# Performance work log

Hardware: AMD Instinct MI355X
Metric: run time of the kernel (lower is better)

## Reference

```python
import jax, jax.numpy as jnp
import numpy as np

NSLICES = 4
HID = 512
IN_FEAT = 342   # input_shape - 1 (last column is phase)
OUT = 311
BATCH = 256


def cubic(y0, y1, y2, y3, mu):
    # Catmull-Rom cubic interpolation, as in the original PFNN code
    return (
        (-0.5 * y0 + 1.5 * y1 - 1.5 * y2 + 0.5 * y3) * mu * mu * mu
        + (y0 - 2.5 * y1 + 2.0 * y2 - 0.5 * y3) * mu * mu
        + (-0.5 * y0 + 0.5 * y2) * mu
        + y1
    )


def setup_inputs() -> dict:
    key = jax.random.key(0)
    ks = jax.random.split(key, 7)
    x = jax.random.uniform(ks[0], (BATCH, IN_FEAT + 1), dtype=jnp.float32)
    s = 0.02
    W0 = jax.random.normal(ks[1], (NSLICES, HID, IN_FEAT), dtype=jnp.float32) * s
    b0 = jax.random.normal(ks[2], (NSLICES, HID), dtype=jnp.float32) * s
    W1 = jax.random.normal(ks[3], (NSLICES, HID, HID), dtype=jnp.float32) * s
    b1 = jax.random.normal(ks[4], (NSLICES, HID), dtype=jnp.float32) * s
    W2 = jax.random.normal(ks[5], (NSLICES, OUT, HID), dtype=jnp.float32) * s
    b2 = jax.random.normal(ks[6], (NSLICES, OUT), dtype=jnp.float32) * s
    return {"x": x, "W0": W0, "b0": b0, "W1": W1, "b1": b1, "W2": W2, "b2": b2}


def reference(x, W0, b0, W1, b1, W2, b2):
    phase = x[:, -1]                       # [B]
    pscale = NSLICES * phase
    mu = jnp.mod(pscale, 1.0)              # [B]
    i1 = jnp.floor(pscale).astype(jnp.int32) % NSLICES
    i0 = (i1 - 1) % NSLICES
    i2 = (i1 + 1) % NSLICES
    i3 = (i1 + 2) % NSLICES
    muW = mu[:, None, None]                # broadcast over (out, in)
    mub = mu[:, None]

    Wb0 = cubic(W0[i0], W0[i1], W0[i2], W0[i3], muW)   # [B, 512, 342]
    bb0 = cubic(b0[i0], b0[i1], b0[i2], b0[i3], mub)   # [B, 512]
    Wb1 = cubic(W1[i0], W1[i1], W1[i2], W1[i3], muW)   # [B, 512, 512]
    bb1 = cubic(b1[i0], b1[i1], b1[i2], b1[i3], mub)
    Wb2 = cubic(W2[i0], W2[i1], W2[i2], W2[i3], muW)   # [B, 311, 512]
    bb2 = cubic(b2[i0], b2[i1], b2[i2], b2[i3], mub)

    h = x[:, :-1]                                       # [B, 342]
    h = jax.nn.elu(jnp.einsum('boi,bi->bo', Wb0, h) + bb0)
    h = jax.nn.elu(jnp.einsum('boi,bi->bo', Wb1, h) + bb1)
    out = jnp.einsum('boi,bi->bo', Wb2, h) + bb2        # [B, 311]
    return out
```

## Files before the change

### kernel.cpp

```cpp
#include <hip/hip_runtime.h>
#include <math.h>

#define NSLICES 4
#define HID 512
#define IN_FEAT 342
#define OUTD 311
#define BATCH 256
#define KP0 352
#define MP2 320
#define XROW (IN_FEAT + 1)

typedef unsigned short u16;
typedef short bf16x8 __attribute__((ext_vector_type(8)));
typedef float f32x4 __attribute__((ext_vector_type(4)));

__device__ __forceinline__ u16 f2bf_rne(float v) {
    unsigned int x = __float_as_uint(v);
    unsigned int r = (x + 0x7fffu + ((x >> 16) & 1u)) >> 16;
    return (u16)r;
}
__device__ __forceinline__ float bf2f(u16 u) {
    return __uint_as_float(((unsigned int)u) << 16);
}

__global__ __launch_bounds__(64) void prep_x(const float* __restrict__ x,
                                             u16* __restrict__ hhi, u16* __restrict__ hlo,
                                             float* __restrict__ dcoef)
{
    const int b = blockIdx.x;
    const float* xr = x + (size_t)b * XROW;
    for (int k = threadIdx.x; k < KP0; k += 64) {
        float v = (k < IN_FEAT) ? xr[k] : 0.f;
        u16 hi = f2bf_rne(v);
        u16 lo = f2bf_rne(v - bf2f(hi));
        hhi[(size_t)b * KP0 + k] = hi;
        hlo[(size_t)b * KP0 + k] = lo;
    }
    if (threadIdx.x == 0) {
        float ps = 4.f * xr[IN_FEAT];
        float fl = floorf(ps);
        float mu = ps - fl;
        int i1 = ((int)fl) & 3;
        float mu2 = mu * mu, mu3 = mu2 * mu;
        float c0 = -0.5f * mu3 + mu2 - 0.5f * mu;
        float c1 = 1.5f * mu3 - 2.5f * mu2 + 1.0f;
        float c2 = -1.5f * mu3 + 2.0f * mu2 + 0.5f * mu;
        float c3 = 0.5f * mu3 - 0.5f * mu2;
        float d[4];
        d[(i1 + 3) & 3] = c0;
        d[i1]           = c1;
        d[(i1 + 1) & 3] = c2;
        d[(i1 + 2) & 3] = c3;
        float* dd = dcoef + b * 4;
        dd[0] = d[0]; dd[1] = d[1]; dd[2] = d[2]; dd[3] = d[3];
    }
}

#define C0 (4 * 512 * 44)
#define C1 (4 * 512 * 64)
#define C2 (4 * 320 * 64)

union U8 { u16 u[8]; uint4 v; };

__global__ __launch_bounds__(256) void prep_w(
    const float* __restrict__ W0, const float* __restrict__ W1, const float* __restrict__ W2,
    u16* __restrict__ whi0, u16* __restrict__ wlo0,
    u16* __restrict__ whi1, u16* __restrict__ wlo1,
    u16* __restrict__ whi2, u16* __restrict__ wlo2)
{
    int i = blockIdx.x * 256 + threadIdx.x;
    float src[8];
    u16* dhi; u16* dlo; size_t doff;
    if (i < C0) {
        int row = i / 44, c = i - row * 44;
        int k = c * 8;
#pragma unroll
        for (int j = 0; j < 8; j++) {
            int kk = k + j;
            src[j] = (kk < IN_FEAT) ? W0[(size_t)row * IN_FEAT + kk] : 0.f;
        }
        dhi = whi0; dlo = wlo0; doff = (size_t)row * KP0 + k;
    } else if (i < C0 + C1) {
        int l = i - C0;
        int row = l >> 6, c = l & 63;
        int k = c * 8;
        const float* p = W1 + (size_t)row * HID + k;
#pragma unroll
        for (int j = 0; j < 8; j++) src[j] = p[j];
        dhi = whi1; dlo = wlo1; doff = (size_t)row * HID + k;
    } else if (i < C0 + C1 + C2) {
        int l = i - C0 - C1;
        int row = l >> 6, c = l & 63;
        int k = c * 8;
        int s = row / 320, o = row - s * 320;
        if (o < OUTD) {
            const float* p = W2 + ((size_t)s * OUTD + o) * HID + k;
#pragma unroll
            for (int j = 0; j < 8; j++) src[j] = p[j];
        } else {
#pragma unroll
            for (int j = 0; j < 8; j++) src[j] = 0.f;
        }
        dhi = whi2; dlo = wlo2; doff = (size_t)row * HID + k;
    } else {
        return;
    }
    U8 hi, lo;
#pragma unroll
    for (int j = 0; j < 8; j++) {
        u16 h = f2bf_rne(src[j]);
        hi.u[j] = h;
        lo.u[j] = f2bf_rne(src[j] - bf2f(h));
    }
    *reinterpret_cast<uint4*>(dhi + doff) = hi.v;
    *reinterpret_cast<uint4*>(dlo + doff) = lo.v;
}

template<int KP, int KLDS>
__global__ __launch_bounds__(256, 2) void gemm_mfma(
    const u16* __restrict__ Whi, const u16* __restrict__ Wlo,
    const u16* __restrict__ Hhi, const u16* __restrict__ Hlo,
    float* __restrict__ Y, int Mp)
{
    __shared__ u16 sHhi[16 * KLDS];
    __shared__ u16 sHlo[16 * KLDS];

    const int tid = (int)threadIdx.x;
    const int b0 = blockIdx.x * 16;
    const int o0 = blockIdx.y * 64;
    const int s  = blockIdx.z;

    constexpr int CH = KP / 8;
    for (int idx = tid; idx < 16 * CH; idx += 256) {
        int r = idx / CH, c = idx - r * CH;
        size_t g = (size_t)(b0 + r) * KP + c * 8;
        *reinterpret_cast<uint4*>(&sHhi[r * KLDS + c * 8]) =
            *reinterpret_cast<const uint4*>(Hhi + g);
        *reinterpret_cast<uint4*>(&sHlo[r * KLDS + c * 8]) =
            *reinterpret_cast<const uint4*>(Hlo + g);
    }
    __syncthreads();

    const int lane = tid & 63;
    const int wv = tid >> 6;
    const int m = lane & 15;
    const int q = lane >> 4;

    const size_t wrow = ((size_t)s * Mp + o0 + wv * 16 + m) * KP + q * 8;
    const u16* wp_hi = Whi + wrow;
    const u16* wp_lo = Wlo + wrow;
    const u16* hp_hi = &sHhi[m * KLDS + q * 8];
    const u16* hp_lo = &sHlo[m * KLDS + q * 8];

    f32x4 acc0 = {0.f, 0.f, 0.f, 0.f};
    f32x4 acc1 = {0.f, 0.f, 0.f, 0.f};
    f32x4 acc2 = {0.f, 0.f, 0.f, 0.f};

#pragma unroll
    for (int c = 0; c < KP / 32; ++c) {
        bf16x8 ah = *reinterpret_cast<const bf16x8*>(wp_hi + c * 32);
        bf16x8 al = *reinterpret_cast<const bf16x8*>(wp_lo + c * 32);
        bf16x8 bh = *reinterpret_cast<const bf16x8*>(hp_hi + c * 32);
        bf16x8 bl = *reinterpret_cast<const bf16x8*>(hp_lo + c * 32);
        acc0 = __builtin_amdgcn_mfma_f32_16x16x32_bf16(ah, bh, acc0, 0, 0, 0);
        acc1 = __builtin_amdgcn_mfma_f32_16x16x32_bf16(ah, bl, acc1, 0, 0, 0);
        acc2 = __builtin_amdgcn_mfma_f32_16x16x32_bf16(al, bh, acc2, 0, 0, 0);
    }

    f32x4 r = acc0 + acc1 + acc2;
    const int b = b0 + m;
    const int ob = o0 + wv * 16 + q * 4;
    float* dst = Y + ((size_t)s * BATCH + b) * Mp + ob;
    *reinterpret_cast<float4*>(dst) = make_float4(r[0], r[1], r[2], r[3]);
}

__global__ __launch_bounds__(256) void blend(
    const float* __restrict__ Y, const float* __restrict__ bias,
    const float* __restrict__ dcoef, int M, int Mp, int mode,
    u16* __restrict__ hhi, u16* __restrict__ hlo, float* __restrict__ out)
{
    const int b = blockIdx.x;
    const float d0 = dcoef[b * 4 + 0];
    const float d1 = dcoef[b * 4 + 1];
    const float d2 = dcoef[b * 4 + 2];
    const float d3 = dcoef[b * 4 + 3];
    const float* yb = Y + (size_t)b * Mp;
    const size_t plane = (size_t)BATCH * Mp;

    for (int o = (int)threadIdx.x; o < M; o += 256) {
        float v = d0 * (yb[0 * plane + o] + bias[0 * M + o])
                + d1 * (yb[1 * plane + o] + bias[1 * M + o])
                + d2 * (yb[2 * plane + o] + bias[2 * M + o])
                + d3 * (yb[3 * plane + o] + bias[3 * M + o]);
        if (mode) {
            v = (v > 0.f) ? v : expm1f(v);
            u16 hi = f2bf_rne(v);
            hhi[(size_t)b * M + o] = hi;
            hlo[(size_t)b * M + o] = f2bf_rne(v - bf2f(hi));
        } else {
            out[(size_t)b * M + o] = v;
        }
    }
}

extern "C" void kernel_launch(void* const* d_in, const int* in_sizes, int n_in,
                              void* d_out, int out_size, void* d_ws, size_t ws_size,
                              hipStream_t stream) {
    const float* x  = (const float*)d_in[0];
    const float* W0 = (const float*)d_in[1];
    const float* b0 = (const float*)d_in[2];
    const float* W1 = (const float*)d_in[3];
    const float* b1 = (const float*)d_in[4];
    const float* W2 = (const float*)d_in[5];
    const float* b2 = (const float*)d_in[6];
    float* out = (float*)d_out;

    char* p = (char*)d_ws;
    auto alloc = [&](size_t bytes) { char* r = p; p += (bytes + 255) & ~(size_t)255; return r; };

    float* dcoef = (float*)alloc(BATCH * 4 * sizeof(float));
    float* Y     = (float*)alloc((size_t)4 * BATCH * HID * sizeof(float));
    u16* whi0 = (u16*)alloc((size_t)4 * HID * KP0 * 2);
    u16* wlo0 = (u16*)alloc((size_t)4 * HID * KP0 * 2);
    u16* whi1 = (u16*)alloc((size_t)4 * HID * HID * 2);
    u16* wlo1 = (u16*)alloc((size_t)4 * HID * HID * 2);
    u16* whi2 = (u16*)alloc((size_t)4 * MP2 * HID * 2);
    u16* wlo2 = (u16*)alloc((size_t)4 * MP2 * HID * 2);
    u16* h0hi = (u16*)alloc((size_t)BATCH * KP0 * 2);
    u16* h0lo = (u16*)alloc((size_t)BATCH * KP0 * 2);
    u16* hahi = (u16*)alloc((size_t)BATCH * HID * 2);
    u16* halo = (u16*)alloc((size_t)BATCH * HID * 2);
    u16* hbhi = (u16*)alloc((size_t)BATCH * HID * 2);
    u16* hblo = (u16*)alloc((size_t)BATCH * HID * 2);

    prep_x<<<dim3(BATCH), 64, 0, stream>>>(x, h0hi, h0lo, dcoef);
    {
        int tot = C0 + C1 + C2;
        prep_w<<<dim3((tot + 255) / 256), 256, 0, stream>>>(
            W0, W1, W2, whi0, wlo0, whi1, wlo1, whi2, wlo2);
    }

    gemm_mfma<KP0, KP0 + 8><<<dim3(BATCH / 16, HID / 64, 4), 256, 0, stream>>>(
        whi0, wlo0, h0hi, h0lo, Y, HID);
    blend<<<dim3(BATCH), 256, 0, stream>>>(Y, b0, dcoef, HID, HID, 1, hahi, halo, nullptr);

    gemm_mfma<HID, HID + 8><<<dim3(BATCH / 16, HID / 64, 4), 256, 0, stream>>>(
        whi1, wlo1, hahi, halo, Y, HID);
    blend<<<dim3(BATCH), 256, 0, stream>>>(Y, b1, dcoef, HID, HID, 1, hbhi, hblo, nullptr);

    gemm_mfma<HID, HID + 8><<<dim3(BATCH / 16, MP2 / 64, 4), 256, 0, stream>>>(
        whi2, wlo2, hbhi, hblo, Y, MP2);
    blend<<<dim3(BATCH), 256, 0, stream>>>(Y, b2, dcoef, OUTD, MP2, 0, nullptr, nullptr, out);
}
```

Measured before the change: 112.6 us.

## Fuse slice blend, bias and ELU into GEMM and merge prep kernels

```diff
diff --git a/kernel.cpp b/kernel.cpp
--- a/kernel.cpp
+++ b/kernel.cpp
@@ -23,21 +23,29 @@
     return __uint_as_float(((unsigned int)u) << 16);
 }
 
-__global__ __launch_bounds__(64) void prep_x(const float* __restrict__ x,
-                                             u16* __restrict__ hhi, u16* __restrict__ hlo,
-                                             float* __restrict__ dcoef)
+#define C0 (4 * 512 * 44)
+#define C1 (4 * 512 * 64)
+#define C2 (4 * 320 * 64)
+#define CX (256 * 44)
+#define PREP_TOT (C0 + C1 + C2 + CX + 256)
+
+union U8 { u16 u[8]; uint4 v; };
+
+__global__ __launch_bounds__(256) void prep_all(
+    const float* __restrict__ x,
+    const float* __restrict__ W0, const float* __restrict__ W1, const float* __restrict__ W2,
+    u16* __restrict__ whi0, u16* __restrict__ wlo0,
+    u16* __restrict__ whi1, u16* __restrict__ wlo1,
+    u16* __restrict__ whi2, u16* __restrict__ wlo2,
+    u16* __restrict__ h0hi, u16* __restrict__ h0lo,
+    float* __restrict__ dcoef)
 {
-    const int b = blockIdx.x;
-    const float* xr = x + (size_t)b * XROW;
-    for (int k = threadIdx.x; k < KP0; k += 64) {
-        float v = (k < IN_FEAT) ? xr[k] : 0.f;
-        u16 hi = f2bf_rne(v);
-        u16 lo = f2bf_rne(v - bf2f(hi));
-        hhi[(size_t)b * KP0 + k] = hi;
-        hlo[(size_t)b * KP0 + k] = lo;
-    }
-    if (threadIdx.x == 0) {
-        float ps = 4.f * xr[IN_FEAT];
+    int i = blockIdx.x * 256 + threadIdx.x;
+    if (i >= PREP_TOT) return;
+
+    if (i >= C0 + C1 + C2 + CX) {
+        int b = i - (C0 + C1 + C2 + CX);
+        float ps = 4.f * x[(size_t)b * XROW + IN_FEAT];
         float fl = floorf(ps);
         float mu = ps - fl;
         int i1 = ((int)fl) & 3;
@@ -51,24 +59,10 @@
         d[i1]           = c1;
         d[(i1 + 1) & 3] = c2;
         d[(i1 + 2) & 3] = c3;
-        float* dd = dcoef + b * 4;
-        dd[0] = d[0]; dd[1] = d[1]; dd[2] = d[2]; dd[3] = d[3];
-    }
-}
-
-#define C0 (4 * 512 * 44)
-#define C1 (4 * 512 * 64)
-#define C2 (4 * 320 * 64)
-
-union U8 { u16 u[8]; uint4 v; };
-
-__global__ __launch_bounds__(256) void prep_w(
-    const float* __restrict__ W0, const float* __restrict__ W1, const float* __restrict__ W2,
-    u16* __restrict__ whi0, u16* __restrict__ wlo0,
-    u16* __restrict__ whi1, u16* __restrict__ wlo1,
-    u16* __restrict__ whi2, u16* __restrict__ wlo2)
-{
-    int i = blockIdx.x * 256 + threadIdx.x;
+        *reinterpret_cast<float4*>(dcoef + b * 4) = make_float4(d[0], d[1], d[2], d[3]);
+        return;
+    }
+
     float src[8];
     u16* dhi; u16* dlo; size_t doff;
     if (i < C0) {
@@ -103,8 +97,17 @@
         }
         dhi = whi2; dlo = wlo2; doff = (size_t)row * HID + k;
     } else {
-        return;
-    }
+        int l = i - C0 - C1 - C2;
+        int b = l / 44, c = l - b * 44;
+        int k = c * 8;
+#pragma unroll
+        for (int j = 0; j < 8; j++) {
+            int kk = k + j;
+            src[j] = (kk < IN_FEAT) ? x[(size_t)b * XROW + kk] : 0.f;
+        }
+        dhi = h0hi; dlo = h0lo; doff = (size_t)b * KP0 + k;
+    }
+
     U8 hi, lo;
 #pragma unroll
     for (int j = 0; j < 8; j++) {
@@ -116,19 +119,20 @@
     *reinterpret_cast<uint4*>(dlo + doff) = lo.v;
 }
 
-template<int KP, int KLDS>
-__global__ __launch_bounds__(256, 2) void gemm_mfma(
+template<int KP, int KLDS, int FINAL>
+__global__ __launch_bounds__(256) void layer_fused(
     const u16* __restrict__ Whi, const u16* __restrict__ Wlo,
     const u16* __restrict__ Hhi, const u16* __restrict__ Hlo,
-    float* __restrict__ Y, int Mp)
+    const float* __restrict__ bias, const float* __restrict__ dcoef,
+    int Mp, int M,
+    u16* __restrict__ Ohi, u16* __restrict__ Olo, float* __restrict__ out)
 {
-    __shared__ u16 sHhi[16 * KLDS];
-    __shared__ u16 sHlo[16 * KLDS];
+    __shared__ __align__(16) u16 sHhi[16 * KLDS];
+    __shared__ __align__(16) u16 sHlo[16 * KLDS];
 
     const int tid = (int)threadIdx.x;
     const int b0 = blockIdx.x * 16;
     const int o0 = blockIdx.y * 64;
-    const int s  = blockIdx.z;
 
     constexpr int CH = KP / 8;
     for (int idx = tid; idx < 16 * CH; idx += 256) {
@@ -145,60 +149,71 @@
     const int wv = tid >> 6;
     const int m = lane & 15;
     const int q = lane >> 4;
-
-    const size_t wrow = ((size_t)s * Mp + o0 + wv * 16 + m) * KP + q * 8;
-    const u16* wp_hi = Whi + wrow;
-    const u16* wp_lo = Wlo + wrow;
+    const int b = b0 + m;
+
+    const float4 dv = *reinterpret_cast<const float4*>(dcoef + b * 4);
+    const float ds[4] = {dv.x, dv.y, dv.z, dv.w};
+
     const u16* hp_hi = &sHhi[m * KLDS + q * 8];
     const u16* hp_lo = &sHlo[m * KLDS + q * 8];
-
-    f32x4 acc0 = {0.f, 0.f, 0.f, 0.f};
-    f32x4 acc1 = {0.f, 0.f, 0.f, 0.f};
-    f32x4 acc2 = {0.f, 0.f, 0.f, 0.f};
-
-#pragma unroll
-    for (int c = 0; c < KP / 32; ++c) {
-        bf16x8 ah = *reinterpret_cast<const bf16x8*>(wp_hi + c * 32);
-        bf16x8 al = *reinterpret_cast<const bf16x8*>(wp_lo + c * 32);
-        bf16x8 bh = *reinterpret_cast<const bf16x8*>(hp_hi + c * 32);
-        bf16x8 bl = *reinterpret_cast<const bf16x8*>(hp_lo + c * 32);
-        acc0 = __builtin_amdgcn_mfma_f32_16x16x32_bf16(ah, bh, acc0, 0, 0, 0);
-        acc1 = __builtin_amdgcn_mfma_f32_16x16x32_bf16(ah, bl, acc1, 0, 0, 0);
-        acc2 = __builtin_amdgcn_mfma_f32_16x16x32_bf16(al, bh, acc2, 0, 0, 0);
-    }
-
-    f32x4 r = acc0 + acc1 + acc2;
-    const int b = b0 + m;
-    const int ob = o0 + wv * 16 + q * 4;
-    float* dst = Y + ((size_t)s * BATCH + b) * Mp + ob;
-    *reinterpret_cast<float4*>(dst) = make_float4(r[0], r[1], r[2], r[3]);
-}
-
-__global__ __launch_bounds__(256) void blend(
-    const float* __restrict__ Y, const float* __restrict__ bias,
-    const float* __restrict__ dcoef, int M, int Mp, int mode,
-    u16* __restrict__ hhi, u16* __restrict__ hlo, float* __restrict__ out)
-{
-    const int b = blockIdx.x;
-    const float d0 = dcoef[b * 4 + 0];
-    const float d1 = dcoef[b * 4 + 1];
-    const float d2 = dcoef[b * 4 + 2];
-    const float d3 = dcoef[b * 4 + 3];
-    const float* yb = Y + (size_t)b * Mp;
-    const size_t plane = (size_t)BATCH * Mp;
-
-    for (int o = (int)threadIdx.x; o < M; o += 256) {
-        float v = d0 * (yb[0 * plane + o] + bias[0 * M + o])
-                + d1 * (yb[1 * plane + o] + bias[1 * M + o])
-                + d2 * (yb[2 * plane + o] + bias[2 * M + o])
-                + d3 * (yb[3 * plane + o] + bias[3 * M + o]);
-        if (mode) {
-            v = (v > 0.f) ? v : expm1f(v);
-            u16 hi = f2bf_rne(v);
-            hhi[(size_t)b * M + o] = hi;
-            hlo[(size_t)b * M + o] = f2bf_rne(v - bf2f(hi));
-        } else {
-            out[(size_t)b * M + o] = v;
+    const size_t wrow0 = ((size_t)(o0 + wv * 16 + m)) * KP + q * 8;
+    const size_t wplane = (size_t)Mp * KP;
+
+    f32x4 bl = {0.f, 0.f, 0.f, 0.f};
+#pragma unroll
+    for (int s = 0; s < 4; ++s) {
+        const u16* wp_hi = Whi + wrow0 + s * wplane;
+        const u16* wp_lo = Wlo + wrow0 + s * wplane;
+        f32x4 a0 = {0.f, 0.f, 0.f, 0.f};
+        f32x4 a1 = {0.f, 0.f, 0.f, 0.f};
+        f32x4 a2 = {0.f, 0.f, 0.f, 0.f};
+#pragma unroll
+        for (int c = 0; c < KP / 32; ++c) {
+            bf16x8 ah = *reinterpret_cast<const bf16x8*>(wp_hi + c * 32);
+            bf16x8 al = *reinterpret_cast<const bf16x8*>(wp_lo + c * 32);
+            bf16x8 bh = *reinterpret_cast<const bf16x8*>(hp_hi + c * 32);
+            bf16x8 b_l = *reinterpret_cast<const bf16x8*>(hp_lo + c * 32);
+            a0 = __builtin_amdgcn_mfma_f32_16x16x32_bf16(ah, bh, a0, 0, 0, 0);
+            a1 = __builtin_amdgcn_mfma_f32_16x16x32_bf16(ah, b_l, a1, 0, 0, 0);
+            a2 = __builtin_amdgcn_mfma_f32_16x16x32_bf16(al, bh, a2, 0, 0, 0);
+        }
+        f32x4 sum = a0 + a1 + a2;
+#pragma unroll
+        for (int r = 0; r < 4; ++r) bl[r] += ds[s] * sum[r];
+    }
+
+    const int obase = o0 + wv * 16 + q * 4;
+    if (!FINAL) {
+        float4 bb0 = *reinterpret_cast<const float4*>(bias + 0 * M + obase);
+        float4 bb1 = *reinterpret_cast<const float4*>(bias + 1 * M + obase);
+        float4 bb2 = *reinterpret_cast<const float4*>(bias + 2 * M + obase);
+        float4 bb3 = *reinterpret_cast<const float4*>(bias + 3 * M + obase);
+        float v[4];
+        v[0] = bl[0] + ds[0]*bb0.x + ds[1]*bb1.x + ds[2]*bb2.x + ds[3]*bb3.x;
+        v[1] = bl[1] + ds[0]*bb0.y + ds[1]*bb1.y + ds[2]*bb2.y + ds[3]*bb3.y;
+        v[2] = bl[2] + ds[0]*bb0.z + ds[1]*bb1.z + ds[2]*bb2.z + ds[3]*bb3.z;
+        v[3] = bl[3] + ds[0]*bb0.w + ds[1]*bb1.w + ds[2]*bb2.w + ds[3]*bb3.w;
+        ushort4 h4, l4;
+        u16* ph = (u16*)&h4; u16* pl = (u16*)&l4;
+#pragma unroll
+        for (int r = 0; r < 4; ++r) {
+            float e = (v[r] > 0.f) ? v[r] : expm1f(v[r]);
+            u16 h = f2bf_rne(e);
+            ph[r] = h;
+            pl[r] = f2bf_rne(e - bf2f(h));
+        }
+        *reinterpret_cast<ushort4*>(Ohi + (size_t)b * M + obase) = h4;
+        *reinterpret_cast<ushort4*>(Olo + (size_t)b * M + obase) = l4;
+    } else {
+        float* dst = out + (size_t)b * M;
+#pragma unroll
+        for (int r = 0; r < 4; ++r) {
+            int o = obase + r;
+            if (o < M) {
+                float bb = ds[0] * bias[0 * M + o] + ds[1] * bias[1 * M + o]
+                         + ds[2] * bias[2 * M + o] + ds[3] * bias[3 * M + o];
+                dst[o] = bl[r] + bb;
+            }
         }
     }
 }
@@ -219,7 +234,6 @@
     auto alloc = [&](size_t bytes) { char* r = p; p += (bytes + 255) & ~(size_t)255; return r; };
 
     float* dcoef = (float*)alloc(BATCH * 4 * sizeof(float));
-    float* Y     = (float*)alloc((size_t)4 * BATCH * HID * sizeof(float));
     u16* whi0 = (u16*)alloc((size_t)4 * HID * KP0 * 2);
     u16* wlo0 = (u16*)alloc((size_t)4 * HID * KP0 * 2);
     u16* whi1 = (u16*)alloc((size_t)4 * HID * HID * 2);
@@ -233,22 +247,15 @@
     u16* hbhi = (u16*)alloc((size_t)BATCH * HID * 2);
     u16* hblo = (u16*)alloc((size_t)BATCH * HID * 2);
 
-    prep_x<<<dim3(BATCH), 64, 0, stream>>>(x, h0hi, h0lo, dcoef);
-    {
-        int tot = C0 + C1 + C2;
-        prep_w<<<dim3((tot + 255) / 256), 256, 0, stream>>>(
-            W0, W1, W2, whi0, wlo0, whi1, wlo1, whi2, wlo2);
-    }
-
-    gemm_mfma<KP0, KP0 + 8><<<dim3(BATCH / 16, HID / 64, 4), 256, 0, stream>>>(
-        whi0, wlo0, h0hi, h0lo, Y, HID);
-    blend<<<dim3(BATCH), 256, 0, stream>>>(Y, b0, dcoef, HID, HID, 1, hahi, halo, nullptr);
-
-    gemm_mfma<HID, HID + 8><<<dim3(BATCH / 16, HID / 64, 4), 256, 0, stream>>>(
-        whi1, wlo1, hahi, halo, Y, HID);
-    blend<<<dim3(BATCH), 256, 0, stream>>>(Y, b1, dcoef, HID, HID, 1, hbhi, hblo, nullptr);
-
-    gemm_mfma<HID, HID + 8><<<dim3(BATCH / 16, MP2 / 64, 4), 256, 0, stream>>>(
-        whi2, wlo2, hbhi, hblo, Y, MP2);
-    blend<<<dim3(BATCH), 256, 0, stream>>>(Y, b2, dcoef, OUTD, MP2, 0, nullptr, nullptr, out);
-}
+    prep_all<<<dim3((PREP_TOT + 255) / 256), 256, 0, stream>>>(
+        x, W0, W1, W2, whi0, wlo0, whi1, wlo1, whi2, wlo2, h0hi, h0lo, dcoef);
+
+    layer_fused<KP0, KP0 + 8, 0><<<dim3(BATCH / 16, HID / 64), 256, 0, stream>>>(
+        whi0, wlo0, h0hi, h0lo, b0, dcoef, HID, HID, hahi, halo, nullptr);
+
+    layer_fused<HID, HID + 8, 0><<<dim3(BATCH / 16, HID / 64), 256, 0, stream>>>(
+        whi1, wlo1, hahi, halo, b1, dcoef, HID, HID, hbhi, hblo, nullptr);
+
+    layer_fused<HID, HID + 8, 1><<<dim3(BATCH / 16, MP2 / 64), 256, 0, stream>>>(
+        whi2, wlo2, hbhi, hblo, b2, dcoef, MP2, OUTD, nullptr, nullptr, out);
+}
```

Result: slower. 129.0 us (+14.6%).
